# Optimization experiments

Hardware: AMD Instinct MI355X
Metric: run time of the kernel (lower is better)

## Reference

```python
import jax, jax.numpy as jnp
import numpy as np

N = 8192
D = 384


def setup_inputs() -> dict:
    key = jax.random.key(0)
    kx, kq, kk, kv, kf = jax.random.split(key, 5)
    x = jax.random.normal(kx, (N, D), dtype=jnp.float32)
    Wq = jax.random.uniform(kq, (D, D), dtype=jnp.float32)
    Wk = jax.random.uniform(kk, (D, D), dtype=jnp.float32)
    Wv = jax.random.uniform(kv, (D, D), dtype=jnp.float32)
    ffws = jax.random.uniform(kf, (D,), dtype=jnp.float32)
    return {"x": x, "Wq": Wq, "Wk": Wk, "Wv": Wv, "ffws": ffws}


def reference(x, Wq, Wk, Wv, ffws):
    def layer(h):
        # Q = Wq @ h.T -> Q.T = h @ Wq.T ; scores = Q.T @ K = (h Wq.T)(Wk h.T)
        Qt = h @ Wq.T                    # [N, D]
        K = Wk @ h.T                     # [D, N]
        scores = jax.nn.softmax(Qt @ K, axis=1)  # [N, N], torch implicit dim=1
        Vt = h @ Wv.T                    # [N, D]
        # weighted_sum double-loop == scores @ Vt (soft_sim is square so
        # choice(size()) always returns N)
        return scores @ Vt               # [N, D]

    z = layer(layer(x))
    # o = sigmoid(sum(ffws * z[-1]))
    return jax.nn.sigmoid(jnp.sum(ffws * z[-1]))
```

## Files before the change

### kernel.cpp

```cpp
#include <hip/hip_runtime.h>
#include <hip/hip_bf16.h>
#include <math.h>

static constexpr int kN = 8192;
static constexpr int kD = 384;
static constexpr int kND = kN * kD;

typedef __attribute__((ext_vector_type(8))) short short8;
typedef __attribute__((ext_vector_type(4))) float f32x4;

__device__ __forceinline__ ushort f2bf(float f) {
  union { float f; unsigned int i; } cv; cv.f = f;
  unsigned int lsb = (cv.i >> 16) & 1u;
  unsigned int r = cv.i + 0x7fffu + lsb;
  return (ushort)(r >> 16);
}
__device__ __forceinline__ float bf2f(ushort u) {
  union { unsigned int i; float f; } cv; cv.i = ((unsigned int)u) << 16;
  return cv.f;
}
__device__ __forceinline__ f32x4 mfma_bf16(short8 a, short8 b, f32x4 c) {
  return __builtin_amdgcn_mfma_f32_16x16x32_bf16(a, b, c, 0, 0, 0);
}
__device__ __forceinline__ void bar_lds() {
  asm volatile("s_waitcnt lgkmcnt(0)" ::: "memory");
  __builtin_amdgcn_s_barrier();
}

__global__ __launch_bounds__(512) void proj_mfma(
    const float* __restrict__ x, const float* __restrict__ Wq,
    const float* __restrict__ Wk, const float* __restrict__ Wv,
    ushort* __restrict__ Qh, ushort* __restrict__ Kh,
    ushort* __restrict__ VTh)
{
  __shared__ ushort XH[128 * 32];
  __shared__ ushort WH[3][96 * 32];

  const int tid = threadIdx.x;
  const int w = tid >> 6;
  const int lane = tid & 63;
  const int l15 = lane & 15;
  const int hi4 = lane >> 4;
  const int i0 = blockIdx.x * 128;
  const int j0 = blockIdx.y * 96;
  const float* Wm[3] = {Wq, Wk, Wv};

  const f32x4 zf = {0.f, 0.f, 0.f, 0.f};
  f32x4 acc[3][6];
#pragma unroll
  for (int m = 0; m < 3; ++m)
#pragma unroll
    for (int ct = 0; ct < 6; ++ct) acc[m][ct] = zf;

  const int xrow = tid >> 2;
  const int xc8 = (tid & 3) * 8;

  for (int dc = 0; dc < 12; ++dc) {
    const int d0 = dc * 32;
    {
      const float* src = x + (size_t)(i0 + xrow) * kD + d0 + xc8;
      const float4 v0 = *reinterpret_cast<const float4*>(src);
      const float4 v1 = *reinterpret_cast<const float4*>(src + 4);
      const float vs[8] = {v0.x, v0.y, v0.z, v0.w, v1.x, v1.y, v1.z, v1.w};
      ushort hh[8];
#pragma unroll
      for (int j = 0; j < 8; ++j) hh[j] = f2bf(vs[j]);
      *reinterpret_cast<uint4*>(&XH[xrow * 32 + xc8]) =
          *reinterpret_cast<const uint4*>(hh);
    }
    if (tid < 384) {
#pragma unroll
      for (int m = 0; m < 3; ++m) {
        const float* src = Wm[m] + (size_t)(j0 + xrow) * kD + d0 + xc8;
        const float4 v0 = *reinterpret_cast<const float4*>(src);
        const float4 v1 = *reinterpret_cast<const float4*>(src + 4);
        const float vs[8] = {v0.x, v0.y, v0.z, v0.w, v1.x, v1.y, v1.z, v1.w};
        ushort hh[8];
#pragma unroll
        for (int j = 0; j < 8; ++j) hh[j] = f2bf(vs[j]);
        *reinterpret_cast<uint4*>(&WH[m][xrow * 32 + xc8]) =
            *reinterpret_cast<const uint4*>(hh);
      }
    }
    __syncthreads();
    const short8 xa = *reinterpret_cast<const short8*>(
        &XH[(16 * w + l15) * 32 + 8 * hi4]);
#pragma unroll
    for (int m = 0; m < 3; ++m) {
#pragma unroll
      for (int ct = 0; ct < 6; ++ct) {
        const short8 wh = *reinterpret_cast<const short8*>(
            &WH[m][(16 * ct + l15) * 32 + 8 * hi4]);
        acc[m][ct] = mfma_bf16(xa, wh, acc[m][ct]);
      }
    }
    __syncthreads();
  }

#pragma unroll
  for (int ct = 0; ct < 6; ++ct)
#pragma unroll
    for (int r = 0; r < 4; ++r) {
      const size_t oi =
          (size_t)(i0 + 16 * w + 4 * hi4 + r) * kD + j0 + 16 * ct + l15;
      Qh[oi] = f2bf(acc[0][ct][r]);
      Kh[oi] = f2bf(acc[1][ct][r]);
    }
#pragma unroll
  for (int ct = 0; ct < 6; ++ct) {
    ushort4 h;
    ushort* hp = &h.x;
#pragma unroll
    for (int r = 0; r < 4; ++r) hp[r] = f2bf(acc[2][ct][r]);
    *reinterpret_cast<ushort4*>(
        &VTh[(size_t)(j0 + 16 * ct + l15) * kN + i0 + 16 * w + 4 * hi4]) = h;
  }
}

static constexpr int SPLITf = 4;
static constexpr int KEYSf = kN / SPLITf;
static constexpr int NTIL = KEYSf / 128;

static constexpr int OFF_QH = 0;
static constexpr int OFF_P  = 50176;

__global__ __launch_bounds__(512, 2) void flash_mfma(
    const ushort* __restrict__ Qh,
    const ushort* __restrict__ Kh,
    const ushort* __restrict__ VTh,
    ushort* __restrict__ Opart, float* __restrict__ ml)
{
  __shared__ ushort LDSU[67584];
  __shared__ float MLB[2048];

  const int tid = threadIdx.x;
  const int w = tid >> 6;
  const int lane = tid & 63;
  const int l15 = lane & 15;
  const int hi4 = lane >> 4;
  const int sp = blockIdx.x;
  const int i0 = blockIdx.y * 128;
  const int kg0 = sp * KEYSf;

  {
    const int row = tid >> 2;
    const int sg = (tid & 3) * 96;
    const ushort* sh = Qh + (size_t)(i0 + row) * kD + sg;
    ushort* dh = LDSU + OFF_QH + row * 392 + sg;
#pragma unroll
    for (int u = 0; u < 12; ++u)
      *reinterpret_cast<uint4*>(dh + 8 * u) =
          *reinterpret_cast<const uint4*>(sh + 8 * u);
  }

  const f32x4 zf = {0.f, 0.f, 0.f, 0.f};
  f32x4 o[8][3];
#pragma unroll
  for (int qt = 0; qt < 8; ++qt)
#pragma unroll
    for (int c = 0; c < 3; ++c) o[qt][c] = zf;
  float m_run[8], l_run[8];
#pragma unroll
  for (int qt = 0; qt < 8; ++qt) { m_run[qt] = -INFINITY; l_run[qt] = 0.f; }

  __syncthreads();

  for (int kb = 0; kb < NTIL; ++kb) {
    const int kg = kg0 + kb * 128;

    f32x4 sacc[8];
#pragma unroll
    for (int qt = 0; qt < 8; ++qt) sacc[qt] = zf;
    const size_t kbase = (size_t)(kg + 16 * w + l15) * kD + 8 * hi4;
    short8 ka[12];
#pragma unroll
    for (int ks = 0; ks < 12; ++ks)
      ka[ks] = *reinterpret_cast<const short8*>(Kh + kbase + 32 * ks);
    __builtin_amdgcn_sched_barrier(0);
#pragma unroll
    for (int ks = 0; ks < 12; ++ks) {
      const int d0 = 32 * ks;
#pragma unroll
      for (int qt = 0; qt < 8; ++qt) {
        const short8 qh = *reinterpret_cast<const short8*>(
            LDSU + OFF_QH + (16 * qt + l15) * 392 + d0 + 8 * hi4);
        sacc[qt] = mfma_bf16(ka[ks], qh, sacc[qt]);
      }
    }

#pragma unroll
    for (int qt = 0; qt < 8; ++qt) {
      float mt = fmaxf(fmaxf(sacc[qt][0], sacc[qt][1]),
                       fmaxf(sacc[qt][2], sacc[qt][3]));
      mt = fmaxf(mt, __shfl_xor(mt, 16, 64));
      mt = fmaxf(mt, __shfl_xor(mt, 32, 64));
      if (lane < 16) MLB[(qt * 16 + l15) * 8 + w] = mt;
    }
    bar_lds();

    short8 vv[12];
#pragma unroll
    for (int c = 0; c < 3; ++c)
#pragma unroll
      for (int kv = 0; kv < 4; ++kv)
        vv[c * 4 + kv] = *reinterpret_cast<const short8*>(
            VTh + (size_t)(48 * w + 16 * c + l15) * kN + kg + 32 * kv + 8 * hi4);
    __builtin_amdgcn_sched_barrier(0);

    float sc[8];
#pragma unroll
    for (int qt = 0; qt < 8; ++qt) {
      const float4 ma =
          *reinterpret_cast<const float4*>(&MLB[(qt * 16 + l15) * 8]);
      const float4 mb =
          *reinterpret_cast<const float4*>(&MLB[(qt * 16 + l15) * 8 + 4]);
      const float Mt = fmaxf(fmaxf(fmaxf(ma.x, ma.y), fmaxf(ma.z, ma.w)),
                             fmaxf(fmaxf(mb.x, mb.y), fmaxf(mb.z, mb.w)));
      const float mnew = fmaxf(m_run[qt], Mt);
      sc[qt] = __expf(m_run[qt] - mnew);
      m_run[qt] = mnew;
      const float p0 = __expf(sacc[qt][0] - mnew);
      const float p1 = __expf(sacc[qt][1] - mnew);
      const float p2 = __expf(sacc[qt][2] - mnew);
      const float p3 = __expf(sacc[qt][3] - mnew);
      float ls = (p0 + p1) + (p2 + p3);
      ls += __shfl_xor(ls, 16, 64);
      ls += __shfl_xor(ls, 32, 64);
      if (lane < 16) MLB[1024 + (qt * 16 + l15) * 8 + w] = ls;
      uint2 HH;
      HH.x = (unsigned int)f2bf(p0) | ((unsigned int)f2bf(p1) << 16);
      HH.y = (unsigned int)f2bf(p2) | ((unsigned int)f2bf(p3) << 16);
      const int pi = (16 * qt + l15) * 136 + 16 * w + 4 * hi4;
      *reinterpret_cast<uint2*>(LDSU + OFF_P + pi) = HH;
#pragma unroll
      for (int r = 0; r < 4; ++r) {
        const float scr_ = __shfl(sc[qt], 4 * hi4 + r, 64);
#pragma unroll
        for (int c = 0; c < 3; ++c) o[qt][c][r] *= scr_;
      }
    }
    bar_lds();
#pragma unroll
    for (int qt = 0; qt < 8; ++qt) {
      const float4 la =
          *reinterpret_cast<const float4*>(&MLB[1024 + (qt * 16 + l15) * 8]);
      const float4 lb =
          *reinterpret_cast<const float4*>(&MLB[1024 + (qt * 16 + l15) * 8 + 4]);
      const float ls = ((la.x + la.y) + (la.z + la.w)) +
                       ((lb.x + lb.y) + (lb.z + lb.w));
      l_run[qt] = l_run[qt] * sc[qt] + ls;
    }

#pragma unroll
    for (int kv = 0; kv < 4; ++kv) {
      short8 pf[8];
#pragma unroll
      for (int qt = 0; qt < 8; ++qt)
        pf[qt] = *reinterpret_cast<const short8*>(
            LDSU + OFF_P + (16 * qt + l15) * 136 + 32 * kv + 8 * hi4);
#pragma unroll
      for (int c = 0; c < 3; ++c) {
#pragma unroll
        for (int qt = 0; qt < 8; ++qt)
          o[qt][c] = mfma_bf16(pf[qt], vv[c * 4 + kv], o[qt][c]);
      }
    }
  }

#pragma unroll
  for (int qt = 0; qt < 8; ++qt) {
    const float linv = 1.0f / l_run[qt];
#pragma unroll
    for (int r = 0; r < 4; ++r) {
      const float lr = __shfl(linv, 4 * hi4 + r, 64);
#pragma unroll
      for (int c = 0; c < 3; ++c)
        Opart[(size_t)sp * kND + (i0 + 16 * qt + 4 * hi4 + r) * kD +
              48 * w + 16 * c + l15] = f2bf(o[qt][c][r] * lr);
    }
  }
  if (w == 0 && lane < 16) {
#pragma unroll
    for (int qt = 0; qt < 8; ++qt) {
      const int mi = (sp * kN + i0 + 16 * qt + l15) * 2;
      ml[mi] = m_run[qt];
      ml[mi + 1] = l_run[qt];
    }
  }
}

__global__ __launch_bounds__(256) void merge_kernel(
    const ushort* __restrict__ Opart, const float* __restrict__ ml,
    float* __restrict__ O)
{
  const size_t idx = (size_t)blockIdx.x * 256 + threadIdx.x;
  const size_t i = idx / kD;
  float m = ml[i * 2];
#pragma unroll
  for (int sp = 1; sp < SPLITf; ++sp)
    m = fmaxf(m, ml[((size_t)sp * kN + i) * 2]);
  float den = 0.f, acc = 0.f;
#pragma unroll
  for (int sp = 0; sp < SPLITf; ++sp) {
    const float e = __expf(ml[((size_t)sp * kN + i) * 2] - m) *
                    ml[((size_t)sp * kN + i) * 2 + 1];
    den += e;
    acc += e * bf2f(Opart[(size_t)sp * kND + idx]);
  }
  O[idx] = acc / den;
}

__global__ __launch_bounds__(64) void qrow_kernel(
    const float* __restrict__ h1, const float* __restrict__ Wq,
    float* __restrict__ q2)
{
  const int j = blockIdx.x;
  const int lane = threadIdx.x;
  const float* hr = h1 + (size_t)(kN - 1) * kD;
  float acc = 0.f;
  for (int d = lane; d < kD; d += 64) acc += hr[d] * Wq[(size_t)j * kD + d];
#pragma unroll
  for (int off = 32; off > 0; off >>= 1) acc += __shfl_xor(acc, off, 64);
  if (lane == 0) q2[j] = acc;
}

__global__ __launch_bounds__(384) void u_kernel(
    const float* __restrict__ Wk, const float* __restrict__ q2,
    float* __restrict__ u)
{
  __shared__ float qs[kD];
  const int d = threadIdx.x;
  qs[d] = q2[d];
  __syncthreads();
  float acc = 0.f;
  for (int k = 0; k < kD; ++k) acc += Wk[(size_t)k * kD + d] * qs[k];
  u[d] = acc;
}

__global__ __launch_bounds__(256) void logits_kernel(
    const float* __restrict__ h1, const float* __restrict__ u,
    float* __restrict__ lg)
{
  const int wave = threadIdx.x >> 6;
  const int lane = threadIdx.x & 63;
  const int j = blockIdx.x * 4 + wave;
  float acc = 0.f;
#pragma unroll
  for (int t = 0; t < kD / 64; ++t) {
    const int d = lane + t * 64;
    acc += h1[(size_t)j * kD + d] * u[d];
  }
#pragma unroll
  for (int off = 32; off > 0; off >>= 1) acc += __shfl_xor(acc, off, 64);
  if (lane == 0) lg[j] = acc;
}

__global__ __launch_bounds__(1024) void smax_kernel(
    const float* __restrict__ lg, float* __restrict__ wgt)
{
  __shared__ float red[16];
  const int t = threadIdx.x;
  const int wave = t >> 6;
  const int lane = t & 63;
  float v[8];
  float mx = -INFINITY;
#pragma unroll
  for (int s = 0; s < 8; ++s) {
    v[s] = lg[t + 1024 * s];
    mx = fmaxf(mx, v[s]);
  }
#pragma unroll
  for (int off = 32; off > 0; off >>= 1) mx = fmaxf(mx, __shfl_xor(mx, off, 64));
  if (lane == 0) red[wave] = mx;
  __syncthreads();
  if (t == 0) {
    float m = red[0];
    for (int i = 1; i < 16; ++i) m = fmaxf(m, red[i]);
    red[0] = m;
  }
  __syncthreads();
  const float m = red[0];
  __syncthreads();
  float sum = 0.f;
#pragma unroll
  for (int s = 0; s < 8; ++s) {
    v[s] = expf(v[s] - m);
    sum += v[s];
  }
#pragma unroll
  for (int off = 32; off > 0; off >>= 1) sum += __shfl_xor(sum, off, 64);
  if (lane == 0) red[wave] = sum;
  __syncthreads();
  if (t == 0) {
    float S = 0.f;
    for (int i = 0; i < 16; ++i) S += red[i];
    red[0] = S;
  }
  __syncthreads();
  const float invS = 1.0f / red[0];
#pragma unroll
  for (int s = 0; s < 8; ++s) wgt[t + 1024 * s] = v[s] * invS;
}

__global__ __launch_bounds__(384) void wsum_kernel(
    const float* __restrict__ wgt, const float* __restrict__ h1,
    float* __restrict__ part)
{
  __shared__ float wl[256];
  const int b = blockIdx.x;
  const int t = threadIdx.x;
  if (t < 256) wl[t] = wgt[b * 256 + t];
  __syncthreads();
  const float* Hp = h1 + (size_t)b * 256 * kD;
  float acc = 0.f;
  for (int j = 0; j < 256; ++j) acc += wl[j] * Hp[(size_t)j * kD + t];
  part[b * kD + t] = acc;
}

__global__ __launch_bounds__(384) void final2_kernel(
    const float* __restrict__ part, const float* __restrict__ Wv,
    const float* __restrict__ ffws, float* __restrict__ out)
{
  __shared__ float zs[kD];
  __shared__ float red[6];
  const int t = threadIdx.x;
  const int wave = t >> 6;
  const int lane = t & 63;
  float z = 0.f;
#pragma unroll
  for (int b = 0; b < 32; ++b) z += part[b * kD + t];
  zs[t] = z;
  __syncthreads();
  float zv = 0.f;
  for (int k = 0; k < kD; ++k) zv += Wv[(size_t)t * kD + k] * zs[k];
  float val = zv * ffws[t];
#pragma unroll
  for (int off = 32; off > 0; off >>= 1) val += __shfl_xor(val, off, 64);
  if (lane == 0) red[wave] = val;
  __syncthreads();
  if (t == 0) {
    float s = red[0];
    for (int i = 1; i < 6; ++i) s += red[i];
    out[0] = 1.0f / (1.0f + expf(-s));
  }
}

extern "C" void kernel_launch(void* const* d_in, const int* in_sizes, int n_in,
                              void* d_out, int out_size, void* d_ws, size_t ws_size,
                              hipStream_t stream) {
  const float* x    = (const float*)d_in[0];
  const float* Wq   = (const float*)d_in[1];
  const float* Wk   = (const float*)d_in[2];
  const float* Wv   = (const float*)d_in[3];
  const float* ffws = (const float*)d_in[4];
  float* out = (float*)d_out;
  char* wsb = (char*)d_ws;

  ushort* Qh  = (ushort*)wsb;
  ushort* Kh  = Qh + kND;
  ushort* VTh = Kh + kND;
  ushort* Opart = VTh + kND;
  float* ml    = (float*)(Opart + (size_t)SPLITf * kND);
  float* h1    = ml + (size_t)SPLITf * kN * 2;
  float* q2    = h1 + (size_t)kND;
  float* u     = q2 + kD;
  float* lg    = u + kD;
  float* wgt   = lg + kN;
  float* part  = wgt + kN;

  proj_mfma<<<dim3(kN / 128, kD / 96), 512, 0, stream>>>(
      x, Wq, Wk, Wv, Qh, Kh, VTh);
  flash_mfma<<<dim3(SPLITf, kN / 128), 512, 0, stream>>>(
      Qh, Kh, VTh, Opart, ml);
  merge_kernel<<<(kN * kD) / 256, 256, 0, stream>>>(Opart, ml, h1);
  qrow_kernel<<<kD, 64, 0, stream>>>(h1, Wq, q2);
  u_kernel<<<1, 384, 0, stream>>>(Wk, q2, u);
  logits_kernel<<<kN / 4, 256, 0, stream>>>(h1, u, lg);
  smax_kernel<<<1, 1024, 0, stream>>>(lg, wgt);
  wsum_kernel<<<32, 384, 0, stream>>>(wgt, h1, part);
  final2_kernel<<<1, 384, 0, stream>>>(part, Wv, ffws, out);
}
```

Measured before the change: 274.1 us.

## Prefetch V earlier in flash loop and widen parallelism of small tail kernels

Moves the V-tile global loads in the flash kernel ahead of the row-max reduction and LDS barrier so their latency overlaps the max computation. The merge kernel is vectorized to process four elements per thread with ushort4/float4 accesses. u_kernel is split across six 64-thread blocks, and wsum_kernel uses 128 blocks of 64 rows instead of 32 blocks of 256 rows, so these small serial kernels use more CUs. The V prefetch holds more registers live across the barrier, and final2 now sums 128 partials per column.

```diff
diff --git a/kernel.cpp b/kernel.cpp
--- a/kernel.cpp
+++ b/kernel.cpp
@@ -187,6 +187,16 @@
         sacc[qt] = mfma_bf16(ka[ks], qh, sacc[qt]);
       }
     }
+    __builtin_amdgcn_sched_barrier(0);
+
+    short8 vv[12];
+#pragma unroll
+    for (int c = 0; c < 3; ++c)
+#pragma unroll
+      for (int kv = 0; kv < 4; ++kv)
+        vv[c * 4 + kv] = *reinterpret_cast<const short8*>(
+            VTh + (size_t)(48 * w + 16 * c + l15) * kN + kg + 32 * kv + 8 * hi4);
+    __builtin_amdgcn_sched_barrier(0);
 
 #pragma unroll
     for (int qt = 0; qt < 8; ++qt) {
@@ -197,15 +207,6 @@
       if (lane < 16) MLB[(qt * 16 + l15) * 8 + w] = mt;
     }
     bar_lds();
-
-    short8 vv[12];
-#pragma unroll
-    for (int c = 0; c < 3; ++c)
-#pragma unroll
-      for (int kv = 0; kv < 4; ++kv)
-        vv[c * 4 + kv] = *reinterpret_cast<const short8*>(
-            VTh + (size_t)(48 * w + 16 * c + l15) * kN + kg + 32 * kv + 8 * hi4);
-    __builtin_amdgcn_sched_barrier(0);
 
     float sc[8];
 #pragma unroll
@@ -293,21 +294,30 @@
     const ushort* __restrict__ Opart, const float* __restrict__ ml,
     float* __restrict__ O)
 {
-  const size_t idx = (size_t)blockIdx.x * 256 + threadIdx.x;
-  const size_t i = idx / kD;
+  const size_t base = ((size_t)blockIdx.x * 256 + threadIdx.x) * 4;
+  const size_t i = base / kD;
   float m = ml[i * 2];
 #pragma unroll
   for (int sp = 1; sp < SPLITf; ++sp)
     m = fmaxf(m, ml[((size_t)sp * kN + i) * 2]);
-  float den = 0.f, acc = 0.f;
+  float den = 0.f;
+  float acc0 = 0.f, acc1 = 0.f, acc2 = 0.f, acc3 = 0.f;
 #pragma unroll
   for (int sp = 0; sp < SPLITf; ++sp) {
     const float e = __expf(ml[((size_t)sp * kN + i) * 2] - m) *
                     ml[((size_t)sp * kN + i) * 2 + 1];
     den += e;
-    acc += e * bf2f(Opart[(size_t)sp * kND + idx]);
-  }
-  O[idx] = acc / den;
+    const ushort4 ov =
+        *reinterpret_cast<const ushort4*>(&Opart[(size_t)sp * kND + base]);
+    acc0 += e * bf2f(ov.x);
+    acc1 += e * bf2f(ov.y);
+    acc2 += e * bf2f(ov.z);
+    acc3 += e * bf2f(ov.w);
+  }
+  const float inv = 1.0f / den;
+  float4 r;
+  r.x = acc0 * inv; r.y = acc1 * inv; r.z = acc2 * inv; r.w = acc3 * inv;
+  *reinterpret_cast<float4*>(&O[base]) = r;
 }
 
 __global__ __launch_bounds__(64) void qrow_kernel(
@@ -324,13 +334,14 @@
   if (lane == 0) q2[j] = acc;
 }
 
-__global__ __launch_bounds__(384) void u_kernel(
+__global__ __launch_bounds__(64) void u_kernel(
     const float* __restrict__ Wk, const float* __restrict__ q2,
     float* __restrict__ u)
 {
   __shared__ float qs[kD];
-  const int d = threadIdx.x;
-  qs[d] = q2[d];
+  const int t = threadIdx.x;
+  const int d = blockIdx.x * 64 + t;
+  for (int k = t; k < kD; k += 64) qs[k] = q2[k];
   __syncthreads();
   float acc = 0.f;
   for (int k = 0; k < kD; ++k) acc += Wk[(size_t)k * kD + d] * qs[k];
@@ -406,14 +417,14 @@
     const float* __restrict__ wgt, const float* __restrict__ h1,
     float* __restrict__ part)
 {
-  __shared__ float wl[256];
+  __shared__ float wl[64];
   const int b = blockIdx.x;
   const int t = threadIdx.x;
-  if (t < 256) wl[t] = wgt[b * 256 + t];
-  __syncthreads();
-  const float* Hp = h1 + (size_t)b * 256 * kD;
+  if (t < 64) wl[t] = wgt[b * 64 + t];
+  __syncthreads();
+  const float* Hp = h1 + (size_t)b * 64 * kD;
   float acc = 0.f;
-  for (int j = 0; j < 256; ++j) acc += wl[j] * Hp[(size_t)j * kD + t];
+  for (int j = 0; j < 64; ++j) acc += wl[j] * Hp[(size_t)j * kD + t];
   part[b * kD + t] = acc;
 }
 
@@ -427,8 +438,7 @@
   const int wave = t >> 6;
   const int lane = t & 63;
   float z = 0.f;
-#pragma unroll
-  for (int b = 0; b < 32; ++b) z += part[b * kD + t];
+  for (int b = 0; b < 128; ++b) z += part[b * kD + t];
   zs[t] = z;
   __syncthreads();
   float zv = 0.f;
@@ -472,11 +482,11 @@
       x, Wq, Wk, Wv, Qh, Kh, VTh);
   flash_mfma<<<dim3(SPLITf, kN / 128), 512, 0, stream>>>(
       Qh, Kh, VTh, Opart, ml);
-  merge_kernel<<<(kN * kD) / 256, 256, 0, stream>>>(Opart, ml, h1);
+  merge_kernel<<<(kN * kD) / 1024, 256, 0, stream>>>(Opart, ml, h1);
   qrow_kernel<<<kD, 64, 0, stream>>>(h1, Wq, q2);
-  u_kernel<<<1, 384, 0, stream>>>(Wk, q2, u);
+  u_kernel<<<kD / 64, 64, 0, stream>>>(Wk, q2, u);
   logits_kernel<<<kN / 4, 256, 0, stream>>>(h1, u, lg);
   smax_kernel<<<1, 1024, 0, stream>>>(lg, wgt);
-  wsum_kernel<<<32, 384, 0, stream>>>(wgt, h1, part);
+  wsum_kernel<<<kN / 64, 384, 0, stream>>>(wgt, h1, part);
   final2_kernel<<<1, 384, 0, stream>>>(part, Wv, ffws, out);
 }
```

Result: faster. 256.5 us, median of 3 (-6.4%).
